# Kernel tuning notes

Measured on AMD Instinct MI355X. Metric: run time of the kernel, lower is better.

The kernel has to match this reference:

```python
import jax, jax.numpy as jnp
import numpy as np

N_NODES = 50000
N_EDGES = 800000
IN_DIM, HID_DIM, NUM_CLASSES = 128, 64, 32
DROP_P = 0.1


def gcn_conv(x, W, b, src, dst, n_nodes):
    """PyG-style GCNConv: x @ W, symmetric normalization with self-loops,
    scatter-add aggregation at dst, then bias. Self-loop contribution is
    added analytically (norm_ii = deg_i^-1) instead of appending edges."""
    h = x @ W  # [N, out]
    deg = jax.ops.segment_sum(jnp.ones((src.shape[0],), h.dtype), dst,
                              num_segments=n_nodes) + 1.0  # +1 for self-loop
    dinv = jax.lax.rsqrt(deg)  # deg >= 1, always finite
    norm = dinv[src] * dinv[dst]  # [E]
    msg = h[src] * norm[:, None]  # gather + scale  [E, out]
    agg = jax.ops.segment_sum(msg, dst, num_segments=n_nodes)
    agg = agg + h * (dinv * dinv)[:, None]  # self-loop term
    return agg + b


def setup_inputs() -> dict:
    key = jax.random.key(0)
    ks = jax.random.split(key, 12)
    x = jax.random.normal(ks[0], (N_NODES, IN_DIM), jnp.float32)
    edge_index = jax.random.randint(ks[1], (2, N_EDGES), 0, N_NODES, jnp.int64)
    # Glorot-ish weights (PyG Linear transform has no bias; bias added post-agg)
    def glorot(k, fan_in, fan_out):
        s = jnp.sqrt(2.0 / (fan_in + fan_out))
        return jax.random.normal(k, (fan_in, fan_out), jnp.float32) * s
    W0 = glorot(ks[2], IN_DIM, HID_DIM)
    b0 = jnp.zeros((HID_DIM,), jnp.float32)
    W1 = glorot(ks[3], HID_DIM, NUM_CLASSES)
    b1 = jnp.zeros((NUM_CLASSES,), jnp.float32)
    W2 = glorot(ks[4], HID_DIM, NUM_CLASSES)
    b2 = jnp.zeros((NUM_CLASSES,), jnp.float32)
    # training-mode randomness, materialized deterministically
    keep = jax.random.bernoulli(ks[5], 1.0 - DROP_P, (N_NODES, HID_DIM))
    dropout_mask = keep.astype(jnp.float32) / (1.0 - DROP_P)
    eps = jax.random.normal(ks[6], (N_NODES, NUM_CLASSES), jnp.float32)
    return {"x": x, "edge_index": edge_index, "W0": W0, "b0": b0,
            "W1": W1, "b1": b1, "W2": W2, "b2": b2,
            "dropout_mask": dropout_mask, "eps": eps}


def reference(x, edge_index, W0, b0, W1, b1, W2, b2, dropout_mask, eps):
    src, dst = edge_index[0], edge_index[1]
    n = x.shape[0]
    h = gcn_conv(x, W0, b0, src, dst, n)
    h = jax.nn.relu(h)
    h = h * dropout_mask  # inverted dropout, training mode
    mu = gcn_conv(h, W1, b1, src, dst, n)
    logvar = gcn_conv(h, W2, b2, src, dst, n)
    # NOTE: source uses std = exp(logvar) (no 0.5 factor)
    z = eps * jnp.exp(logvar) + mu
    return (z, mu, logvar)
```

## Files before the change

kernel.cpp:

```cpp
#include <hip/hip_runtime.h>

#define IN_DIM 128
#define HID 64
#define NC 32
#define SCAN_TILE 2048

__global__ void hist_kernel(const int* __restrict__ dst, int* __restrict__ deg, int E) {
    int e = blockIdx.x * blockDim.x + threadIdx.x;
    if (e < E) atomicAdd(&deg[dst[e]], 1);
}

__global__ __launch_bounds__(256) void scan_tile_kernel(const int* __restrict__ in,
                                                        int* __restrict__ out,
                                                        int* __restrict__ partials, int n) {
    __shared__ int tsum[256];
    int t = threadIdx.x;
    int base = blockIdx.x * SCAN_TILE + t * 8;
    int v[8];
    int s = 0;
    #pragma unroll
    for (int j = 0; j < 8; ++j) {
        int idx = base + j;
        int x = (idx < n) ? in[idx] : 0;
        s += x;
        v[j] = s;
    }
    tsum[t] = s;
    __syncthreads();
    for (int off = 1; off < 256; off <<= 1) {
        int add = (t >= off) ? tsum[t - off] : 0;
        __syncthreads();
        tsum[t] += add;
        __syncthreads();
    }
    int excl = tsum[t] - s;
    #pragma unroll
    for (int j = 0; j < 8; ++j) {
        int idx = base + j;
        if (idx < n) out[idx] = v[j] + excl;
    }
    if (t == 255) partials[blockIdx.x] = tsum[255];
}

__global__ void scan_partials_kernel(int* __restrict__ partials, int nb) {
    if (threadIdx.x == 0 && blockIdx.x == 0) {
        int run = 0;
        for (int b = 0; b < nb; ++b) { int x = partials[b]; partials[b] = run; run += x; }
    }
}

__global__ void rowptr_kernel(const int* __restrict__ scan_buf, const int* __restrict__ partials,
                              int* __restrict__ rowptr, int n) {
    int i = blockIdx.x * blockDim.x + threadIdx.x;
    if (i < n) rowptr[i + 1] = scan_buf[i] + partials[i / SCAN_TILE];
    if (i == 0) rowptr[0] = 0;
}

__global__ void dinv_kernel(const int* __restrict__ deg, float* __restrict__ dinv, int n) {
    int i = blockIdx.x * blockDim.x + threadIdx.x;
    if (i < n) dinv[i] = rsqrtf((float)deg[i] + 1.0f);
}

__global__ void scatter_kernel(const int* __restrict__ src, const int* __restrict__ dst,
                               const float* __restrict__ dinv, const int* __restrict__ rowptr,
                               int* __restrict__ cursor, int2* __restrict__ e_meta, int E) {
    int e = blockIdx.x * blockDim.x + threadIdx.x;
    if (e >= E) return;
    int s = src[e], d = dst[e];
    int pos = rowptr[d] + atomicAdd(&cursor[d], 1);
    float nm = dinv[s] * dinv[d];
    e_meta[pos] = make_int2(s, __float_as_int(nm));
}

__global__ __launch_bounds__(256) void gemm0_kernel(const float* __restrict__ x,
                                                    const float* __restrict__ W,
                                                    float* __restrict__ h0, int n) {
    __shared__ float Ws[IN_DIM * HID];
    __shared__ float xs[16][IN_DIM];
    int tid = threadIdx.x;
    const float4* W4 = (const float4*)W;
    float4* Ws4 = (float4*)Ws;
    #pragma unroll
    for (int j = 0; j < 8; ++j) Ws4[tid + 256 * j] = W4[tid + 256 * j];
    int base = blockIdx.x * 16;
    const float4* x4 = (const float4*)(x + (size_t)base * IN_DIM);
    float4* xs4 = (float4*)xs;
    #pragma unroll
    for (int j = 0; j < 2; ++j) {
        int i = tid + 256 * j;
        if (base + (i >> 5) < n) xs4[i] = x4[i];
    }
    __syncthreads();
    int r = tid >> 4;
    int c4 = (tid & 15) * 4;
    int row = base + r;
    if (row >= n) return;
    float4 acc = make_float4(0.f, 0.f, 0.f, 0.f);
    #pragma unroll
    for (int k = 0; k < IN_DIM; ++k) {
        float xv = xs[r][k];
        float4 w = *(const float4*)&Ws[k * HID + c4];
        acc.x += xv * w.x; acc.y += xv * w.y; acc.z += xv * w.z; acc.w += xv * w.w;
    }
    *(float4*)&h0[(size_t)row * HID + c4] = acc;
}

__global__ __launch_bounds__(256) void gather0_kernel(const int* __restrict__ rowptr,
                                                      const int2* __restrict__ e_meta,
                                                      const float* __restrict__ h0,
                                                      const float* __restrict__ dinv,
                                                      const float* __restrict__ b0,
                                                      const float* __restrict__ mask,
                                                      float* __restrict__ h, int n) {
    int v = blockIdx.x * 4 + (threadIdx.x >> 6);
    int c = threadIdx.x & 63;
    if (v >= n) return;
    int start = rowptr[v], end = rowptr[v + 1];
    float acc = 0.f;
    for (int p = start; p < end; p += 8) {
        int2 mm[8]; float ww[8];
        #pragma unroll
        for (int i = 0; i < 8; ++i) {
            int q = p + i;
            int qi = q < end ? q : end - 1;
            mm[i] = e_meta[qi];
            ww[i] = (q < end) ? __int_as_float(mm[i].y) : 0.f;
        }
        float gg[8];
        #pragma unroll
        for (int i = 0; i < 8; ++i) gg[i] = h0[(size_t)mm[i].x * HID + c];
        #pragma unroll
        for (int i = 0; i < 8; ++i) acc += gg[i] * ww[i];
    }
    float dv = dinv[v];
    float val = acc + h0[(size_t)v * HID + c] * dv * dv + b0[c];
    val = val > 0.f ? val : 0.f;
    h[(size_t)v * HID + c] = val * mask[(size_t)v * HID + c];
}

__global__ __launch_bounds__(256) void gather2_kernel(const int* __restrict__ rowptr,
                                                      const int2* __restrict__ e_meta,
                                                      const float* __restrict__ h,
                                                      float* __restrict__ agg2, int n) {
    int v = blockIdx.x * 4 + (threadIdx.x >> 6);
    int c = threadIdx.x & 63;
    if (v >= n) return;
    int start = rowptr[v], end = rowptr[v + 1];
    float acc = 0.f;
    for (int p = start; p < end; p += 8) {
        int2 mm[8]; float ww[8];
        #pragma unroll
        for (int i = 0; i < 8; ++i) {
            int q = p + i;
            int qi = q < end ? q : end - 1;
            mm[i] = e_meta[qi];
            ww[i] = (q < end) ? __int_as_float(mm[i].y) : 0.f;
        }
        float gg[8];
        #pragma unroll
        for (int i = 0; i < 8; ++i) gg[i] = h[(size_t)mm[i].x * HID + c];
        #pragma unroll
        for (int i = 0; i < 8; ++i) acc += gg[i] * ww[i];
    }
    agg2[(size_t)v * HID + c] = acc;
}

__global__ __launch_bounds__(256) void gemm2_kernel(const float* __restrict__ h,
                                                    const float* __restrict__ agg2,
                                                    const float* __restrict__ dinv,
                                                    const float* __restrict__ W1,
                                                    const float* __restrict__ W2,
                                                    const float* __restrict__ b1,
                                                    const float* __restrict__ b2,
                                                    const float* __restrict__ eps,
                                                    float* __restrict__ zout,
                                                    float* __restrict__ muout,
                                                    float* __restrict__ lvout, int n) {
    __shared__ float W1s[HID * NC];
    __shared__ float W2s[HID * NC];
    __shared__ float Ss[16][HID];
    int tid = threadIdx.x;
    const float4* W14 = (const float4*)W1;
    const float4* W24 = (const float4*)W2;
    float4* W1s4 = (float4*)W1s;
    float4* W2s4 = (float4*)W2s;
    #pragma unroll
    for (int j = 0; j < 2; ++j) {
        W1s4[tid + 256 * j] = W14[tid + 256 * j];
        W2s4[tid + 256 * j] = W24[tid + 256 * j];
    }
    int base = blockIdx.x * 16;
    {
        int row = base + (tid >> 4);
        int cc = (tid & 15) * 4;
        if (row < n) {
            float dv = dinv[row];
            float dv2 = dv * dv;
            float4 hv = *(const float4*)&h[(size_t)row * HID + cc];
            float4 av = *(const float4*)&agg2[(size_t)row * HID + cc];
            float4 s;
            s.x = av.x + dv2 * hv.x; s.y = av.y + dv2 * hv.y;
            s.z = av.z + dv2 * hv.z; s.w = av.w + dv2 * hv.w;
            *(float4*)&Ss[tid >> 4][cc] = s;
        }
    }
    __syncthreads();
    int r = tid >> 4;
    int q = tid & 15;
    int head = q >> 3;
    int c4 = (q & 7) * 4;
    int row = base + r;
    if (row >= n) return;
    const float* Wp = head ? W2s : W1s;
    float4 acc = make_float4(0.f, 0.f, 0.f, 0.f);
    #pragma unroll
    for (int k = 0; k < HID; ++k) {
        float xv = Ss[r][k];
        float4 w = *(const float4*)&Wp[k * NC + c4];
        acc.x += xv * w.x; acc.y += xv * w.y; acc.z += xv * w.z; acc.w += xv * w.w;
    }
    const float* bb = head ? b2 : b1;
    acc.x += bb[c4]; acc.y += bb[c4 + 1]; acc.z += bb[c4 + 2]; acc.w += bb[c4 + 3];
    int lane = threadIdx.x & 63;
    float4 other;
    other.x = __shfl(acc.x, lane ^ 8);
    other.y = __shfl(acc.y, lane ^ 8);
    other.z = __shfl(acc.z, lane ^ 8);
    other.w = __shfl(acc.w, lane ^ 8);
    size_t o = (size_t)row * NC + c4;
    if (head == 0) {
        *(float4*)&muout[o] = acc;
        float4 ev = *(const float4*)&eps[o];
        float4 z;
        z.x = ev.x * expf(other.x) + acc.x;
        z.y = ev.y * expf(other.y) + acc.y;
        z.z = ev.z * expf(other.z) + acc.z;
        z.w = ev.w * expf(other.w) + acc.w;
        *(float4*)&zout[o] = z;
    } else {
        *(float4*)&lvout[o] = acc;
    }
}

extern "C" void kernel_launch(void* const* d_in, const int* in_sizes, int n_in,
                              void* d_out, int out_size, void* d_ws, size_t ws_size,
                              hipStream_t stream) {
    const float* x    = (const float*)d_in[0];
    const int*   ei   = (const int*)d_in[1];
    const float* W0   = (const float*)d_in[2];
    const float* b0   = (const float*)d_in[3];
    const float* W1   = (const float*)d_in[4];
    const float* b1   = (const float*)d_in[5];
    const float* W2   = (const float*)d_in[6];
    const float* b2   = (const float*)d_in[7];
    const float* mask = (const float*)d_in[8];
    const float* eps  = (const float*)d_in[9];

    int n = in_sizes[0] / IN_DIM;
    int E = in_sizes[1] / 2;
    const int* src = ei;
    const int* dst = ei + E;

    int*   ws_i    = (int*)d_ws;
    int*   deg_i   = ws_i;
    int*   cursor  = deg_i + 50048;
    int*   rowptr  = cursor + 50048;
    int*   scanbuf = rowptr + 50056;
    int*   partials= scanbuf + 50048;
    float* dinv    = (float*)(partials + 64);
    int2*  e_meta  = (int2*)(dinv + 50048);
    float* h0      = (float*)(e_meta + E);
    float* h       = h0 + (size_t)n * HID;
    float* agg2    = h + (size_t)n * HID;

    float* zout  = (float*)d_out;
    float* muout = zout + (size_t)n * NC;
    float* lvout = muout + (size_t)n * NC;

    int nb = (n + SCAN_TILE - 1) / SCAN_TILE;

    hipMemsetAsync(deg_i, 0, 2 * 50048 * sizeof(int), stream);

    hist_kernel<<<(E + 255) / 256, 256, 0, stream>>>(dst, deg_i, E);
    scan_tile_kernel<<<nb, 256, 0, stream>>>(deg_i, scanbuf, partials, n);
    scan_partials_kernel<<<1, 64, 0, stream>>>(partials, nb);
    rowptr_kernel<<<(n + 255) / 256, 256, 0, stream>>>(scanbuf, partials, rowptr, n);
    dinv_kernel<<<(n + 255) / 256, 256, 0, stream>>>(deg_i, dinv, n);
    gemm0_kernel<<<(n + 15) / 16, 256, 0, stream>>>(x, W0, h0, n);
    scatter_kernel<<<(E + 255) / 256, 256, 0, stream>>>(src, dst, dinv, rowptr, cursor, e_meta, E);
    gather0_kernel<<<(n + 3) / 4, 256, 0, stream>>>(rowptr, e_meta, h0, dinv, b0, mask, h, n);
    gather2_kernel<<<(n + 3) / 4, 256, 0, stream>>>(rowptr, e_meta, h, agg2, n);
    gemm2_kernel<<<(n + 15) / 16, 256, 0, stream>>>(h, agg2, dinv, W1, W2, b1, b2, eps,
                                                    zout, muout, lvout, n);
}
```

Baseline: 303.6 us.

## Factor edge norm into node-side scaling, store features as bf16, reuse hist rank

Factors the symmetric edge normalization so each source row is pre-scaled by dinv in the producing kernel and each aggregate is post-scaled by dinv. Edge metadata then shrinks from int2 (src plus weight) to a plain int src index. Intermediate hidden features are stored as bf16, halving gather traffic, and the histogram's atomic return value serves as the CSR rank, so the scatter pass needs no second atomic and no cursor buffer. Rounding features to bf16 loses precision, which may exceed tolerance.

```diff
diff --git a/kernel.cpp b/kernel.cpp
--- a/kernel.cpp
+++ b/kernel.cpp
@@ -5,9 +5,19 @@
 #define NC 32
 #define SCAN_TILE 2048
 
-__global__ void hist_kernel(const int* __restrict__ dst, int* __restrict__ deg, int E) {
+__device__ __forceinline__ unsigned short f2bf(float f) {
+    unsigned b = __float_as_uint(f);
+    unsigned r = (b + 0x7FFFu + ((b >> 16) & 1u)) >> 16;
+    return (unsigned short)r;
+}
+__device__ __forceinline__ float bf2f(unsigned short u) {
+    return __uint_as_float(((unsigned)u) << 16);
+}
+
+__global__ void hist_kernel(const int* __restrict__ dst, int* __restrict__ deg,
+                            int* __restrict__ rank, int E) {
     int e = blockIdx.x * blockDim.x + threadIdx.x;
-    if (e < E) atomicAdd(&deg[dst[e]], 1);
+    if (e < E) rank[e] = atomicAdd(&deg[dst[e]], 1);
 }
 
 __global__ __launch_bounds__(256) void scan_tile_kernel(const int* __restrict__ in,
@@ -62,19 +72,18 @@
 }
 
 __global__ void scatter_kernel(const int* __restrict__ src, const int* __restrict__ dst,
-                               const float* __restrict__ dinv, const int* __restrict__ rowptr,
-                               int* __restrict__ cursor, int2* __restrict__ e_meta, int E) {
+                               const int* __restrict__ rank, const int* __restrict__ rowptr,
+                               int* __restrict__ e_src, int E) {
     int e = blockIdx.x * blockDim.x + threadIdx.x;
     if (e >= E) return;
-    int s = src[e], d = dst[e];
-    int pos = rowptr[d] + atomicAdd(&cursor[d], 1);
-    float nm = dinv[s] * dinv[d];
-    e_meta[pos] = make_int2(s, __float_as_int(nm));
+    int d = dst[e];
+    e_src[rowptr[d] + rank[e]] = src[e];
 }
 
 __global__ __launch_bounds__(256) void gemm0_kernel(const float* __restrict__ x,
                                                     const float* __restrict__ W,
-                                                    float* __restrict__ h0, int n) {
+                                                    const float* __restrict__ dinv,
+                                                    unsigned short* __restrict__ hp0, int n) {
     __shared__ float Ws[IN_DIM * HID];
     __shared__ float xs[16][IN_DIM];
     int tid = threadIdx.x;
@@ -102,71 +111,73 @@
         float4 w = *(const float4*)&Ws[k * HID + c4];
         acc.x += xv * w.x; acc.y += xv * w.y; acc.z += xv * w.z; acc.w += xv * w.w;
     }
-    *(float4*)&h0[(size_t)row * HID + c4] = acc;
+    float dv = dinv[row];
+    ushort4 o;
+    o.x = f2bf(acc.x * dv); o.y = f2bf(acc.y * dv);
+    o.z = f2bf(acc.z * dv); o.w = f2bf(acc.w * dv);
+    *(ushort4*)&hp0[(size_t)row * HID + c4] = o;
 }
 
 __global__ __launch_bounds__(256) void gather0_kernel(const int* __restrict__ rowptr,
-                                                      const int2* __restrict__ e_meta,
-                                                      const float* __restrict__ h0,
+                                                      const int* __restrict__ e_src,
+                                                      const unsigned short* __restrict__ hp0,
                                                       const float* __restrict__ dinv,
                                                       const float* __restrict__ b0,
                                                       const float* __restrict__ mask,
-                                                      float* __restrict__ h, int n) {
+                                                      unsigned short* __restrict__ hb, int n) {
     int v = blockIdx.x * 4 + (threadIdx.x >> 6);
     int c = threadIdx.x & 63;
     if (v >= n) return;
     int start = rowptr[v], end = rowptr[v + 1];
     float acc = 0.f;
     for (int p = start; p < end; p += 8) {
-        int2 mm[8]; float ww[8];
+        int ss[8];
         #pragma unroll
         for (int i = 0; i < 8; ++i) {
             int q = p + i;
-            int qi = q < end ? q : end - 1;
-            mm[i] = e_meta[qi];
-            ww[i] = (q < end) ? __int_as_float(mm[i].y) : 0.f;
+            ss[i] = e_src[q < end ? q : end - 1];
         }
-        float gg[8];
-        #pragma unroll
-        for (int i = 0; i < 8; ++i) gg[i] = h0[(size_t)mm[i].x * HID + c];
-        #pragma unroll
-        for (int i = 0; i < 8; ++i) acc += gg[i] * ww[i];
+        unsigned short gu[8];
+        #pragma unroll
+        for (int i = 0; i < 8; ++i) gu[i] = hp0[(size_t)ss[i] * HID + c];
+        #pragma unroll
+        for (int i = 0; i < 8; ++i) acc += (p + i < end) ? bf2f(gu[i]) : 0.f;
     }
     float dv = dinv[v];
-    float val = acc + h0[(size_t)v * HID + c] * dv * dv + b0[c];
+    float selfv = bf2f(hp0[(size_t)v * HID + c]);
+    float val = dv * (acc + selfv) + b0[c];
     val = val > 0.f ? val : 0.f;
-    h[(size_t)v * HID + c] = val * mask[(size_t)v * HID + c];
+    val = val * mask[(size_t)v * HID + c] * dv;
+    hb[(size_t)v * HID + c] = f2bf(val);
 }
 
 __global__ __launch_bounds__(256) void gather2_kernel(const int* __restrict__ rowptr,
-                                                      const int2* __restrict__ e_meta,
-                                                      const float* __restrict__ h,
-                                                      float* __restrict__ agg2, int n) {
+                                                      const int* __restrict__ e_src,
+                                                      const unsigned short* __restrict__ hb,
+                                                      float* __restrict__ T, int n) {
     int v = blockIdx.x * 4 + (threadIdx.x >> 6);
     int c = threadIdx.x & 63;
     if (v >= n) return;
     int start = rowptr[v], end = rowptr[v + 1];
     float acc = 0.f;
     for (int p = start; p < end; p += 8) {
-        int2 mm[8]; float ww[8];
+        int ss[8];
         #pragma unroll
         for (int i = 0; i < 8; ++i) {
             int q = p + i;
-            int qi = q < end ? q : end - 1;
-            mm[i] = e_meta[qi];
-            ww[i] = (q < end) ? __int_as_float(mm[i].y) : 0.f;
+            ss[i] = e_src[q < end ? q : end - 1];
         }
-        float gg[8];
-        #pragma unroll
-        for (int i = 0; i < 8; ++i) gg[i] = h[(size_t)mm[i].x * HID + c];
-        #pragma unroll
-        for (int i = 0; i < 8; ++i) acc += gg[i] * ww[i];
-    }
-    agg2[(size_t)v * HID + c] = acc;
-}
-
-__global__ __launch_bounds__(256) void gemm2_kernel(const float* __restrict__ h,
-                                                    const float* __restrict__ agg2,
+        unsigned short gu[8];
+        #pragma unroll
+        for (int i = 0; i < 8; ++i) gu[i] = hb[(size_t)ss[i] * HID + c];
+        #pragma unroll
+        for (int i = 0; i < 8; ++i) acc += (p + i < end) ? bf2f(gu[i]) : 0.f;
+    }
+    acc += bf2f(hb[(size_t)v * HID + c]);
+    T[(size_t)v * HID + c] = acc;
+}
+
+__global__ __launch_bounds__(256) void gemm2_kernel(const float* __restrict__ T,
                                                     const float* __restrict__ dinv,
                                                     const float* __restrict__ W1,
                                                     const float* __restrict__ W2,
@@ -195,12 +206,9 @@
         int cc = (tid & 15) * 4;
         if (row < n) {
             float dv = dinv[row];
-            float dv2 = dv * dv;
-            float4 hv = *(const float4*)&h[(size_t)row * HID + cc];
-            float4 av = *(const float4*)&agg2[(size_t)row * HID + cc];
+            float4 tv = *(const float4*)&T[(size_t)row * HID + cc];
             float4 s;
-            s.x = av.x + dv2 * hv.x; s.y = av.y + dv2 * hv.y;
-            s.z = av.z + dv2 * hv.z; s.w = av.w + dv2 * hv.w;
+            s.x = dv * tv.x; s.y = dv * tv.y; s.z = dv * tv.z; s.w = dv * tv.w;
             *(float4*)&Ss[tid >> 4][cc] = s;
         }
     }
@@ -263,15 +271,15 @@
 
     int*   ws_i    = (int*)d_ws;
     int*   deg_i   = ws_i;
-    int*   cursor  = deg_i + 50048;
-    int*   rowptr  = cursor + 50048;
+    int*   rowptr  = deg_i + 50048;
     int*   scanbuf = rowptr + 50056;
     int*   partials= scanbuf + 50048;
     float* dinv    = (float*)(partials + 64);
-    int2*  e_meta  = (int2*)(dinv + 50048);
-    float* h0      = (float*)(e_meta + E);
-    float* h       = h0 + (size_t)n * HID;
-    float* agg2    = h + (size_t)n * HID;
+    int*   rank    = (int*)(dinv + 50048);
+    int*   e_src   = rank + E;
+    unsigned short* hp0 = (unsigned short*)(e_src + E);
+    unsigned short* hb  = hp0 + (size_t)n * HID;
+    float* T       = (float*)(hb + (size_t)n * HID);
 
     float* zout  = (float*)d_out;
     float* muout = zout + (size_t)n * NC;
@@ -279,17 +287,17 @@
 
     int nb = (n + SCAN_TILE - 1) / SCAN_TILE;
 
-    hipMemsetAsync(deg_i, 0, 2 * 50048 * sizeof(int), stream);
-
-    hist_kernel<<<(E + 255) / 256, 256, 0, stream>>>(dst, deg_i, E);
+    hipMemsetAsync(deg_i, 0, 50048 * sizeof(int), stream);
+
+    hist_kernel<<<(E + 255) / 256, 256, 0, stream>>>(dst, deg_i, rank, E);
     scan_tile_kernel<<<nb, 256, 0, stream>>>(deg_i, scanbuf, partials, n);
     scan_partials_kernel<<<1, 64, 0, stream>>>(partials, nb);
     rowptr_kernel<<<(n + 255) / 256, 256, 0, stream>>>(scanbuf, partials, rowptr, n);
     dinv_kernel<<<(n + 255) / 256, 256, 0, stream>>>(deg_i, dinv, n);
-    gemm0_kernel<<<(n + 15) / 16, 256, 0, stream>>>(x, W0, h0, n);
-    scatter_kernel<<<(E + 255) / 256, 256, 0, stream>>>(src, dst, dinv, rowptr, cursor, e_meta, E);
-    gather0_kernel<<<(n + 3) / 4, 256, 0, stream>>>(rowptr, e_meta, h0, dinv, b0, mask, h, n);
-    gather2_kernel<<<(n + 3) / 4, 256, 0, stream>>>(rowptr, e_meta, h, agg2, n);
-    gemm2_kernel<<<(n + 15) / 16, 256, 0, stream>>>(h, agg2, dinv, W1, W2, b1, b2, eps,
+    gemm0_kernel<<<(n + 15) / 16, 256, 0, stream>>>(x, W0, dinv, hp0, n);
+    scatter_kernel<<<(E + 255) / 256, 256, 0, stream>>>(src, dst, rank, rowptr, e_src, E);
+    gather0_kernel<<<(n + 3) / 4, 256, 0, stream>>>(rowptr, e_src, hp0, dinv, b0, mask, hb, n);
+    gather2_kernel<<<(n + 3) / 4, 256, 0, stream>>>(rowptr, e_src, hb, T, n);
+    gemm2_kernel<<<(n + 15) / 16, 256, 0, stream>>>(T, dinv, W1, W2, b1, b2, eps,
                                                     zout, muout, lvout, n);
 }
```

Result: faster. 262.9 us (-13.4%).
